# Optimization experiments

Measured on AMD Instinct MI355X. Metric: run time of the kernel, lower is better.

The kernel has to match this reference:

```python
import jax, jax.numpy as jnp
import numpy as np

B, N, X_DIM, Y_DIM = 256, 128, 8, 8
Z_DIM, R_DIM, HID = 64, 128, 256
STEPS = 50
SIGMA_SQ = 0.5 ** 2
EPSILON = 1.0


def setup_inputs() -> dict:
    key = jax.random.key(0)
    ks = jax.random.split(key, 20)
    s = lambda fan_in: 1.0 / np.sqrt(fan_in)
    inp = {
        'x_ctx': jax.random.normal(ks[0], (B, N, X_DIM), jnp.float32),
        'y_ctx': jax.random.normal(ks[1], (B, N, Y_DIM), jnp.float32),
        'mask': jnp.ones((B, N, 1), jnp.float32),
        'z0': jax.random.normal(ks[2], (B, Z_DIM), jnp.float32),
        'noise': jax.random.normal(ks[3], (STEPS, B, Z_DIM), jnp.float32),
        # encoder: pointwise MLP on [x,y] then masked mean pool, project to r_dim
        'We1': jax.random.normal(ks[4], (X_DIM + Y_DIM, HID), jnp.float32) * s(X_DIM + Y_DIM),
        'be1': jnp.zeros((HID,), jnp.float32),
        'We2': jax.random.normal(ks[5], (HID, R_DIM), jnp.float32) * s(HID),
        'be2': jnp.zeros((R_DIM,), jnp.float32),
        # decoder: MLP([x, z]) -> y per context point
        'Wd1': jax.random.normal(ks[6], (X_DIM + Z_DIM, HID), jnp.float32) * s(X_DIM + Z_DIM),
        'bd1': jnp.zeros((HID,), jnp.float32),
        'Wd2': jax.random.normal(ks[7], (HID, Y_DIM), jnp.float32) * s(HID),
        'bd2': jnp.zeros((Y_DIM,), jnp.float32),
        # drift net: MLP([z, r, t]) -> z_dim
        'Wb1': jax.random.normal(ks[8], (Z_DIM + R_DIM + 1, HID), jnp.float32) * s(Z_DIM + R_DIM + 1),
        'bb1': jnp.zeros((HID,), jnp.float32),
        'Wb2': jax.random.normal(ks[9], (HID, Z_DIM), jnp.float32) * s(HID),
        'bb2': jnp.zeros((Z_DIM,), jnp.float32),
    }
    return inp


def _encode(x, y, mask, We1, be1, We2, be2):
    phi = jax.nn.gelu(jnp.concatenate([x, y], axis=-1) @ We1 + be1)  # [B,N,H]
    pooled = (phi * mask).sum(axis=1) / jnp.maximum(mask.sum(axis=1), 1.0)  # [B,H]
    return pooled @ We2 + be2  # [B,R]


def _decode(z, x, Wd1, bd1, Wd2, bd2):
    zb = jnp.broadcast_to(z[:, None, :], (z.shape[0], x.shape[1], z.shape[1]))
    h = jax.nn.gelu(jnp.concatenate([x, zb], axis=-1) @ Wd1 + bd1)  # [B,N,H]
    return h @ Wd2 + bd2  # [B,N,Y]


def _drift(z, r, t_col, Wb1, bb1, Wb2, bb2):
    h = jax.nn.gelu(jnp.concatenate([z, r, t_col], axis=-1) @ Wb1 + bb1)
    return h @ Wb2 + bb2  # [B,Z]


def reference(x_ctx, y_ctx, mask, z0, noise,
              We1, be1, We2, be2, Wd1, bd1, Wd2, bd2, Wb1, bb1, Wb2, bb2):
    dt = 1.0 / STEPS
    r = _encode(x_ctx, y_ctx, mask, We1, be1, We2, be2)  # [B,R]

    def energy_sum(z, t):
        u0 = 0.5 * jnp.sum(z ** 2, axis=1)  # [B]
        mu_y = _decode(z, x_ctx, Wd1, bd1, Wd2, bd2)
        sse = jnp.sum(((y_ctx - mu_y) ** 2) * mask, axis=(1, 2))  # [B]
        u1 = 0.5 * sse / SIGMA_SQ + u0
        return jnp.sum((1.0 - t) * u0 + t * u1)

    grad_energy = jax.grad(energy_sum, argnums=0)
    t_steps = (jnp.arange(STEPS, dtype=jnp.float32) * dt)
    noise_scale = jnp.sqrt(jnp.float32(2.0 * EPSILON * dt))

    def step(z, xs):
        t_curr, eps_noise = xs
        grad_u = jnp.clip(grad_energy(z, t_curr), -100.0, 100.0)
        t_col = jnp.full((z.shape[0], 1), t_curr, dtype=z.dtype)
        b = _drift(z, r, t_col, Wb1, bb1, Wb2, bb2)
        dz = (-EPSILON * grad_u + b) * dt + noise_scale * eps_noise
        return z + dz, None

    z_final, _ = jax.lax.scan(step, z0, (t_steps, noise))
    return z_final
```

## Files before the change

kernel.cpp:

```cpp
#include <hip/hip_runtime.h>
#include <math.h>

#define BB    256
#define NN_   128
#define ZD    64
#define RD    128
#define HID   256
#define NSTEPS 50
#define NT    16
#define NTILES 8
#define TPB   1024
#define PADD  258
#define SPLIT 25

__device__ __forceinline__ double fast_exp_d(double x) {
    const double L2E   = 1.44269504088896340736;
    const double LN2HI = 6.93147180369123816490e-01;
    const double LN2LO = 1.90821492927058770002e-10;
    const double MAGIC = 6755399441055744.0;
    double vn = fma(x, L2E, MAGIC);
    int ni = __double2loint(vn);
    double n = vn - MAGIC;
    double r = fma(n, -LN2HI, x);
    r = fma(n, -LN2LO, r);
    double r2 = r * r;
    double r4 = r2 * r2;
    double p01 = 1.0 + r;
    double p23 = fma(r, 1.66666666666666666667e-01, 0.5);
    double p45 = fma(r, 8.33333333333333333333e-03, 4.16666666666666666667e-02);
    double p67 = fma(r, 1.98412698412698412698e-04, 1.38888888888888888889e-03);
    double p89 = fma(r, 2.75573192239858906526e-06, 2.48015873015873015873e-05);
    double pAB = fma(r, 2.50521083854417187751e-08, 2.75573192239858906526e-07);
    double q0 = fma(r2, p23, p01);
    double q1 = fma(r2, p67, p45);
    double q2 = fma(r2, pAB, p89);
    double p = fma(r4, fma(r4, q2, q1), q0);
    return p * __hiloint2double((1023 + ni) << 20, 0);
}

__device__ __forceinline__ double sigmoid_d(double w) {
    double wc = fmin(fmax(w, -60.0), 60.0);
    double e = fast_exp_d(-wc);
    double d = 1.0 + e;
    float r0 = __builtin_amdgcn_rcpf((float)d);
    double y = (double)r0;
    y = fma(y, fma(-d, y, 1.0), y);
    y = fma(y, fma(-d, y, 1.0), y);
    return y;
}

__device__ __forceinline__ double gelu_d(double x) {
    const double c2 = 1.59576912160573071176;
    double w = c2 * x * fma(0.044715, x * x, 1.0);
    return x * sigmoid_d(w);
}

__device__ __forceinline__ void gelu_both_d(double x, double& h, double& gp) {
    const double c  = 0.79788456080286535588;
    const double a  = 0.044715;
    double x2 = x * x;
    double w  = (2.0 * c) * x * fma(a, x2, 1.0);
    double hp = sigmoid_d(w);
    h = x * hp;
    double s = hp * (1.0 - hp);
    gp = fma(x * s, (2.0 * c) * fma(3.0 * a, x2, 1.0), hp);
}

__device__ __forceinline__ void gelu_both_f(float x, float& h, float& gp) {
    const float c2 = 1.5957691216f;
    float x2 = x * x;
    float w  = c2 * x * fmaf(0.044715f, x2, 1.0f);
    float e  = __expf(-w);
    float d  = 1.0f + e;
    float r0 = __builtin_amdgcn_rcpf(d);
    float hp = r0 * fmaf(-d, r0, 2.0f);
    h = x * hp;
    float sg = hp * (1.0f - hp);
    gp = fmaf(x * sg, c2 * fmaf(0.134145f, x2, 1.0f), hp);
}

__device__ __forceinline__ float gelu_f32(float x) {
    const float c2 = 1.5957691216f;
    float w  = c2 * x * fmaf(0.044715f, x * x, 1.0f);
    float e  = __expf(-w);
    float d  = 1.0f + e;
    float r0 = __builtin_amdgcn_rcpf(d);
    float hp = r0 * fmaf(-d, r0, 2.0f);
    return x * hp;
}

struct Smem {
    double h_t[NT][PADD];
    float  wd2t_f[8][PADD];
    double z_ds[ZD];
    double hb_ds[HID];
    double scratch4[4][HID];
    double pmgz[1024];
    double res_r[NT][8];
    double bp_d[16][ZD];
    double bd2_d[8];
    double bb2_d[ZD];
    double hbt_s[HID];
    double wbt_s[HID];
    float  bd1_s[HID];
    float  x_s[NN_][8];
    float  y_s[NN_][8];
    float  m_s[NN_];
    float  z_f[ZD];
    float  hb_f[HID];
    __align__(16) float4 wd1z4[HID][16];
};

__global__ void __launch_bounds__(TPB)
nets_sampler_kernel(
    const float* __restrict__ x_ctx, const float* __restrict__ y_ctx,
    const float* __restrict__ mask,  const float* __restrict__ z0,
    const float* __restrict__ noise,
    const float* __restrict__ We1, const float* __restrict__ be1,
    const float* __restrict__ We2, const float* __restrict__ be2,
    const float* __restrict__ Wd1, const float* __restrict__ bd1,
    const float* __restrict__ Wd2, const float* __restrict__ bd2,
    const float* __restrict__ Wb1, const float* __restrict__ bb1,
    const float* __restrict__ Wb2, const float* __restrict__ bb2,
    float* __restrict__ out)
{
    extern __shared__ char smem_raw[];
    Smem& sm = *reinterpret_cast<Smem*>(smem_raw);

    const int b   = blockIdx.x;
    const int tid = threadIdx.x;
    const int j   = tid & 255;
    const int q2  = tid >> 8;
    const int du_k = tid & 63, du_c = tid >> 6;
    double* r_d = &sm.res_r[0][0];

    if (tid < 256) {
        reinterpret_cast<float4*>(&sm.x_s[0][0])[tid] =
            reinterpret_cast<const float4*>(x_ctx + (size_t)b * NN_ * 8)[tid];
        reinterpret_cast<float4*>(&sm.y_s[0][0])[tid] =
            reinterpret_cast<const float4*>(y_ctx + (size_t)b * NN_ * 8)[tid];
        sm.bd1_s[j] = bd1[j];
        float4 a0 = reinterpret_cast<const float4*>(Wd2 + (size_t)j * 8)[0];
        float4 a1 = reinterpret_cast<const float4*>(Wd2 + (size_t)j * 8)[1];
        sm.wd2t_f[0][j] = a0.x; sm.wd2t_f[1][j] = a0.y;
        sm.wd2t_f[2][j] = a0.z; sm.wd2t_f[3][j] = a0.w;
        sm.wd2t_f[4][j] = a1.x; sm.wd2t_f[5][j] = a1.y;
        sm.wd2t_f[6][j] = a1.z; sm.wd2t_f[7][j] = a1.w;
    }
    if (tid < NN_) sm.m_s[tid] = mask[(size_t)b * NN_ + tid];
    if (tid < ZD) {
        float zf = z0[(size_t)b * ZD + tid];
        sm.z_ds[tid]  = (double)zf;
        sm.z_f[tid]   = zf;
        sm.bb2_d[tid] = (double)bb2[tid];
    }
    if (tid < 8) sm.bd2_d[tid] = (double)bd2[tid];

#pragma unroll
    for (int kk = 0; kk < 16; kk++) {
        const int k = q2 * 16 + kk;
        const float v = Wd1[(8 + k) * HID + j];
        reinterpret_cast<float*>(&sm.wd1z4[j][0])[4 * ((k >> 2) ^ (j & 15)) + (k & 3)] = v;
    }

    float wd1x[8];
#pragma unroll
    for (int k = 0; k < 8; k++) wd1x[k] = Wd1[k * HID + j];

    __syncthreads();

    if (tid < 256) {
        float we1r[16];
#pragma unroll
        for (int k = 0; k < 16; k++) we1r[k] = We1[k * HID + j];
        double be1_d = (double)be1[j];
        double msum = 0.0;
        for (int n = 0; n < NN_; n++) msum += (double)sm.m_s[n];
        msum = fmax(msum, 1.0);
        double pacc = 0.0;
        for (int n = 0; n < NN_; n++) {
            double pre = be1_d;
#pragma unroll
            for (int k = 0; k < 8; k++) pre = fma((double)sm.x_s[n][k], (double)we1r[k], pre);
#pragma unroll
            for (int k = 0; k < 8; k++) pre = fma((double)sm.y_s[n][k], (double)we1r[8 + k], pre);
            pacc += gelu_d(pre) * (double)sm.m_s[n];
        }
        sm.hb_ds[j] = pacc / msum;
    }
    __syncthreads();
    if (tid < 256) {
        int i = tid & 127, half = tid >> 7;
        double racc = 0.0;
        for (int jj = half * 128; jj < half * 128 + 128; jj++)
            racc = fma(sm.hb_ds[jj], (double)We2[jj * RD + i], racc);
        sm.scratch4[half][i] = racc;
    }
    __syncthreads();
    if (tid < RD) r_d[tid] = sm.scratch4[0][tid] + sm.scratch4[1][tid] + (double)be2[tid];
    __syncthreads();

    if (tid < 256) {
        double hbr = (double)bb1[j];
        for (int k = 0; k < RD; k++)
            hbr = fma(r_d[k], (double)Wb1[(ZD + k) * HID + j], hbr);
        sm.hbt_s[j] = hbr;
        sm.wbt_s[j] = (double)Wb1[(ZD + RD) * HID + j];
    }
    __syncthreads();

    const double dt  = 1.0 / (double)NSTEPS;
    const double nsc = sqrt(2.0 * 1.0 * dt);

    float* h_f   = reinterpret_cast<float*>(&sm.h_t[0][0]);
    float* res_f = reinterpret_cast<float*>(&sm.res_r[0][0]);
    float* pm_f  = reinterpret_cast<float*>(&sm.pmgz[0]);

    for (int s = 0; s < SPLIT; s++) {
        const double t = (double)s * dt;

        float nzf = 0.0f;
        if (tid < ZD) nzf = noise[((size_t)s * BB + b) * ZD + tid];

        {
            const int kb = q2 * 16;
            const float* wb1p = Wb1 + kb * HID + j;
            double a0 = 0.0;
#pragma unroll 8
            for (int kk = 0; kk < 16; kk++)
                a0 = fma(sm.z_ds[kb + kk], (double)wb1p[kk * HID], a0);
            sm.scratch4[q2][j] = a0;

            double zq0 = 0.0, zq1 = 0.0;
#pragma unroll
            for (int q = q2 * 4; q < q2 * 4 + 4; q++) {
                float4 wv = sm.wd1z4[j][q ^ (j & 15)];
                const int k = q * 4;
                zq0 = fma(sm.z_ds[k],     (double)wv.x, zq0);
                zq1 = fma(sm.z_ds[k + 1], (double)wv.y, zq1);
                zq0 = fma(sm.z_ds[k + 2], (double)wv.z, zq0);
                zq1 = fma(sm.z_ds[k + 3], (double)wv.w, zq1);
            }
            sm.pmgz[q2 * 256 + j] = zq0 + zq1;
        }
        __syncthreads();
        if (tid < 256) {
            double hacc = sm.hbt_s[j] + t * sm.wbt_s[j]
                        + sm.scratch4[0][j] + sm.scratch4[1][j]
                        + sm.scratch4[2][j] + sm.scratch4[3][j];
            sm.hb_ds[j] = gelu_d(hacc);
        }
        __syncthreads();
        {
            const float* wb2p = Wb2 + (du_c * 16) * ZD + du_k;
            double acc = 0.0;
#pragma unroll 8
            for (int i = 0; i < 16; i++)
                acc = fma(sm.hb_ds[du_c * 16 + i], (double)wb2p[i * ZD], acc);
            sm.bp_d[du_c][du_k] = acc;
        }

        if (s > 0) {
            const double zpre = (double)sm.bd1_s[j]
                + ((sm.pmgz[j] + sm.pmgz[256 + j]) + (sm.pmgz[512 + j] + sm.pmgz[768 + j]));
            const int rb = q2 * 4;

            float gp_r0, gp_r1, gp_r2, gp_r3;
            double T0 = 0.0, T1 = 0.0, T2 = 0.0, T3 = 0.0;
            double T4 = 0.0, T5 = 0.0, T6 = 0.0, T7 = 0.0;

            for (int tile = 0; tile < NTILES; tile++) {
                const int xb = tile * NT + rb;
                {
                    const float4 xa = *reinterpret_cast<const float4*>(&sm.x_s[xb + 0][0]);
                    const float4 xxb = *reinterpret_cast<const float4*>(&sm.x_s[xb + 0][4]);
                    const float4 xc = *reinterpret_cast<const float4*>(&sm.x_s[xb + 1][0]);
                    const float4 xd = *reinterpret_cast<const float4*>(&sm.x_s[xb + 1][4]);
                    double p0 = zpre, p1 = zpre;
                    p0 = fma((double)xa.x, (double)wd1x[0], p0);
                    p0 = fma((double)xa.y, (double)wd1x[1], p0);
                    p0 = fma((double)xa.z, (double)wd1x[2], p0);
                    p0 = fma((double)xa.w, (double)wd1x[3], p0);
                    p0 = fma((double)xxb.x, (double)wd1x[4], p0);
                    p0 = fma((double)xxb.y, (double)wd1x[5], p0);
                    p0 = fma((double)xxb.z, (double)wd1x[6], p0);
                    p0 = fma((double)xxb.w, (double)wd1x[7], p0);
                    p1 = fma((double)xc.x, (double)wd1x[0], p1);
                    p1 = fma((double)xc.y, (double)wd1x[1], p1);
                    p1 = fma((double)xc.z, (double)wd1x[2], p1);
                    p1 = fma((double)xc.w, (double)wd1x[3], p1);
                    p1 = fma((double)xd.x, (double)wd1x[4], p1);
                    p1 = fma((double)xd.y, (double)wd1x[5], p1);
                    p1 = fma((double)xd.z, (double)wd1x[6], p1);
                    p1 = fma((double)xd.w, (double)wd1x[7], p1);
                    double h0, g0, h1, g1;
                    gelu_both_d(p0, h0, g0);
                    gelu_both_d(p1, h1, g1);
                    sm.h_t[rb + 0][j] = h0; gp_r0 = (float)g0;
                    sm.h_t[rb + 1][j] = h1; gp_r1 = (float)g1;
                }
                {
                    const float4 xa = *reinterpret_cast<const float4*>(&sm.x_s[xb + 2][0]);
                    const float4 xxb = *reinterpret_cast<const float4*>(&sm.x_s[xb + 2][4]);
                    const float4 xc = *reinterpret_cast<const float4*>(&sm.x_s[xb + 3][0]);
                    const float4 xd = *reinterpret_cast<const float4*>(&sm.x_s[xb + 3][4]);
                    double p0 = zpre, p1 = zpre;
                    p0 = fma((double)xa.x, (double)wd1x[0], p0);
                    p0 = fma((double)xa.y, (double)wd1x[1], p0);
                    p0 = fma((double)xa.z, (double)wd1x[2], p0);
                    p0 = fma((double)xa.w, (double)wd1x[3], p0);
                    p0 = fma((double)xxb.x, (double)wd1x[4], p0);
                    p0 = fma((double)xxb.y, (double)wd1x[5], p0);
                    p0 = fma((double)xxb.z, (double)wd1x[6], p0);
                    p0 = fma((double)xxb.w, (double)wd1x[7], p0);
                    p1 = fma((double)xc.x, (double)wd1x[0], p1);
                    p1 = fma((double)xc.y, (double)wd1x[1], p1);
                    p1 = fma((double)xc.z, (double)wd1x[2], p1);
                    p1 = fma((double)xc.w, (double)wd1x[3], p1);
                    p1 = fma((double)xd.x, (double)wd1x[4], p1);
                    p1 = fma((double)xd.y, (double)wd1x[5], p1);
                    p1 = fma((double)xd.z, (double)wd1x[6], p1);
                    p1 = fma((double)xd.w, (double)wd1x[7], p1);
                    double h0, g0, h1, g1;
                    gelu_both_d(p0, h0, g0);
                    gelu_both_d(p1, h1, g1);
                    sm.h_t[rb + 2][j] = h0; gp_r2 = (float)g0;
                    sm.h_t[rb + 3][j] = h1; gp_r3 = (float)g1;
                }
                __syncthreads();
                {
                    const int q = tid >> 7, pair = tid & 127;
                    const int nn = pair >> 3, yd = pair & 7;
                    const double2* hrow = reinterpret_cast<const double2*>(&sm.h_t[nn][q * 32]);
                    const float2*  wrow = reinterpret_cast<const float2*>(&sm.wd2t_f[yd][q * 32]);
                    double a0 = 0.0, a1 = 0.0;
#pragma unroll 8
                    for (int i = 0; i < 16; i++) {
                        double2 hv = hrow[i];
                        float2  wv = wrow[i];
                        a0 = fma(hv.x, (double)wv.x, a0);
                        a1 = fma(hv.y, (double)wv.y, a1);
                    }
                    sm.pmgz[q * 128 + pair] = a0 + a1;
                }
                __syncthreads();
                if (tid < 128) {
                    const int nn = tid >> 3, yd = tid & 7;
                    double mu = sm.bd2_d[yd];
#pragma unroll
                    for (int q = 0; q < 8; q++) mu += sm.pmgz[q * 128 + tid];
                    sm.res_r[nn][yd] = 4.0 * t * (mu - (double)sm.y_s[tile * NT + nn][yd])
                                               * (double)sm.m_s[tile * NT + nn];
                }
                __syncthreads();
                {
                    const double2* rr0 = reinterpret_cast<const double2*>(&sm.res_r[rb + 0][0]);
                    const double2* rr1 = reinterpret_cast<const double2*>(&sm.res_r[rb + 1][0]);
                    const double2* rr2 = reinterpret_cast<const double2*>(&sm.res_r[rb + 2][0]);
                    const double2* rr3 = reinterpret_cast<const double2*>(&sm.res_r[rb + 3][0]);
                    double2 a0, a1, a2, a3;
                    double g;
                    g = (double)gp_r0;
                    a0 = rr0[0]; a1 = rr0[1]; a2 = rr0[2]; a3 = rr0[3];
                    T0 = fma(a0.x, g, T0); T1 = fma(a0.y, g, T1);
                    T2 = fma(a1.x, g, T2); T3 = fma(a1.y, g, T3);
                    T4 = fma(a2.x, g, T4); T5 = fma(a2.y, g, T5);
                    T6 = fma(a3.x, g, T6); T7 = fma(a3.y, g, T7);
                    g = (double)gp_r1;
                    a0 = rr1[0]; a1 = rr1[1]; a2 = rr1[2]; a3 = rr1[3];
                    T0 = fma(a0.x, g, T0); T1 = fma(a0.y, g, T1);
                    T2 = fma(a1.x, g, T2); T3 = fma(a1.y, g, T3);
                    T4 = fma(a2.x, g, T4); T5 = fma(a2.y, g, T5);
                    T6 = fma(a3.x, g, T6); T7 = fma(a3.y, g, T7);
                    g = (double)gp_r2;
                    a0 = rr2[0]; a1 = rr2[1]; a2 = rr2[2]; a3 = rr2[3];
                    T0 = fma(a0.x, g, T0); T1 = fma(a0.y, g, T1);
                    T2 = fma(a1.x, g, T2); T3 = fma(a1.y, g, T3);
                    T4 = fma(a2.x, g, T4); T5 = fma(a2.y, g, T5);
                    T6 = fma(a3.x, g, T6); T7 = fma(a3.y, g, T7);
                    g = (double)gp_r3;
                    a0 = rr3[0]; a1 = rr3[1]; a2 = rr3[2]; a3 = rr3[3];
                    T0 = fma(a0.x, g, T0); T1 = fma(a0.y, g, T1);
                    T2 = fma(a1.x, g, T2); T3 = fma(a1.y, g, T3);
                    T4 = fma(a2.x, g, T4); T5 = fma(a2.y, g, T5);
                    T6 = fma(a3.x, g, T6); T7 = fma(a3.y, g, T7);
                }
            }
            {
                double S = T0 * (double)sm.wd2t_f[0][j];
                S = fma(T1, (double)sm.wd2t_f[1][j], S);
                S = fma(T2, (double)sm.wd2t_f[2][j], S);
                S = fma(T3, (double)sm.wd2t_f[3][j], S);
                S = fma(T4, (double)sm.wd2t_f[4][j], S);
                S = fma(T5, (double)sm.wd2t_f[5][j], S);
                S = fma(T6, (double)sm.wd2t_f[6][j], S);
                S = fma(T7, (double)sm.wd2t_f[7][j], S);
                sm.scratch4[q2][j] = S;
            }
            __syncthreads();
            {
                const int k = du_k, c = du_c;
                const int qk = k >> 2, ck = k & 3;
                double acc = 0.0;
#pragma unroll 8
                for (int i = 0; i < 16; i++) {
                    const int jj = c * 16 + i;
                    const float w = reinterpret_cast<const float*>(&sm.wd1z4[jj][0])
                                        [4 * (qk ^ (jj & 15)) + ck];
                    const double sv = sm.scratch4[0][jj] + sm.scratch4[1][jj]
                                    + sm.scratch4[2][jj] + sm.scratch4[3][jj];
                    acc = fma(sv, (double)w, acc);
                }
                sm.pmgz[c * 64 + k] = acc;
            }
            __syncthreads();
        } else {
            __syncthreads();
        }

        if (tid < ZD) {
            double gsum = sm.z_ds[tid];
            if (s > 0) {
#pragma unroll
                for (int c = 0; c < 16; c++) gsum += sm.pmgz[c * 64 + tid];
            }
            gsum = fmin(fmax(gsum, -100.0), 100.0);
            double bdr = sm.bb2_d[tid];
#pragma unroll
            for (int c = 0; c < 16; c++) bdr += sm.bp_d[c][tid];
            double znew = sm.z_ds[tid] + (bdr - gsum) * dt + nsc * (double)nzf;
            sm.z_ds[tid] = znew;
            sm.z_f[tid]  = (float)znew;
        }
        __syncthreads();
    }

    for (int s = SPLIT; s < NSTEPS; s++) {
        const double t = (double)s * dt;

        float nzf = 0.0f;
        if (tid < ZD) nzf = noise[((size_t)s * BB + b) * ZD + tid];

        {
            const int kb = q2 * 16;
            const float* wb1p = Wb1 + kb * HID + j;
            float a0f = 0.0f;
#pragma unroll 8
            for (int kk = 0; kk < 16; kk++)
                a0f = fmaf(sm.z_f[kb + kk], wb1p[kk * HID], a0f);
            sm.scratch4[q2][j] = (double)a0f;

            double zq0 = 0.0, zq1 = 0.0;
#pragma unroll
            for (int q = q2 * 4; q < q2 * 4 + 4; q++) {
                float4 wv = sm.wd1z4[j][q ^ (j & 15)];
                const int k = q * 4;
                zq0 = fma(sm.z_ds[k],     (double)wv.x, zq0);
                zq1 = fma(sm.z_ds[k + 1], (double)wv.y, zq1);
                zq0 = fma(sm.z_ds[k + 2], (double)wv.z, zq0);
                zq1 = fma(sm.z_ds[k + 3], (double)wv.w, zq1);
            }
            sm.pmgz[q2 * 256 + j] = zq0 + zq1;
        }
        __syncthreads();
        if (tid < 256) {
            double hacc = sm.hbt_s[j] + t * sm.wbt_s[j]
                        + sm.scratch4[0][j] + sm.scratch4[1][j]
                        + sm.scratch4[2][j] + sm.scratch4[3][j];
            sm.hb_f[j] = gelu_f32((float)hacc);
        }
        __syncthreads();
        {
            const float* wb2p = Wb2 + (du_c * 16) * ZD + du_k;
            float accf = 0.0f;
#pragma unroll 8
            for (int i = 0; i < 16; i++)
                accf = fmaf(sm.hb_f[du_c * 16 + i], wb2p[i * ZD], accf);
            sm.bp_d[du_c][du_k] = (double)accf;
        }

        const double zpre = (double)sm.bd1_s[j]
            + ((sm.pmgz[j] + sm.pmgz[256 + j]) + (sm.pmgz[512 + j] + sm.pmgz[768 + j]));
        const float zpre_f = (float)zpre;
        const int rb2 = q2 * 8;

        float gpA, gpB, gpC, gpD, gpE, gpF2, gpG, gpH;
        float T0 = 0.f, T1 = 0.f, T2 = 0.f, T3 = 0.f;
        float T4 = 0.f, T5 = 0.f, T6 = 0.f, T7 = 0.f;

        for (int tile = 0; tile < 4; tile++) {
            const int xb = tile * 32 + rb2;
#define FPAIR(RO, GA, GB) { \
            const float4 xa = *reinterpret_cast<const float4*>(&sm.x_s[xb + (RO)][0]); \
            const float4 xbv = *reinterpret_cast<const float4*>(&sm.x_s[xb + (RO)][4]); \
            const float4 xc = *reinterpret_cast<const float4*>(&sm.x_s[xb + (RO) + 1][0]); \
            const float4 xdv = *reinterpret_cast<const float4*>(&sm.x_s[xb + (RO) + 1][4]); \
            float p0 = zpre_f, p1 = zpre_f; \
            p0 = fmaf(xa.x, wd1x[0], p0);  p0 = fmaf(xa.y, wd1x[1], p0); \
            p0 = fmaf(xa.z, wd1x[2], p0);  p0 = fmaf(xa.w, wd1x[3], p0); \
            p0 = fmaf(xbv.x, wd1x[4], p0); p0 = fmaf(xbv.y, wd1x[5], p0); \
            p0 = fmaf(xbv.z, wd1x[6], p0); p0 = fmaf(xbv.w, wd1x[7], p0); \
            p1 = fmaf(xc.x, wd1x[0], p1);  p1 = fmaf(xc.y, wd1x[1], p1); \
            p1 = fmaf(xc.z, wd1x[2], p1);  p1 = fmaf(xc.w, wd1x[3], p1); \
            p1 = fmaf(xdv.x, wd1x[4], p1); p1 = fmaf(xdv.y, wd1x[5], p1); \
            p1 = fmaf(xdv.z, wd1x[6], p1); p1 = fmaf(xdv.w, wd1x[7], p1); \
            float h0, g0, h1, g1; \
            gelu_both_f(p0, h0, g0); \
            gelu_both_f(p1, h1, g1); \
            h_f[(rb2 + (RO)) * PADD + j]     = h0; \
            h_f[(rb2 + (RO) + 1) * PADD + j] = h1; \
            GA = g0; GB = g1; }
            FPAIR(0, gpA, gpB)
            FPAIR(2, gpC, gpD)
            FPAIR(4, gpE, gpF2)
            FPAIR(6, gpG, gpH)
#undef FPAIR
            __syncthreads();
#pragma unroll
            for (int it = 0; it < 2; it++) {
                const int slot = tid + it * 1024;
                const int q = slot >> 8, pair = slot & 255;
                const int nn = pair >> 3, yd = pair & 7;
                const float2* hrow =
                    reinterpret_cast<const float2*>(h_f + nn * PADD) + q * 16;
                const float2* wrow =
                    reinterpret_cast<const float2*>(&sm.wd2t_f[yd][0]) + q * 16;
                float a0 = 0.f, a1 = 0.f;
#pragma unroll 8
                for (int i = 0; i < 16; i++) {
                    float2 hv = hrow[i];
                    float2 wv = wrow[i];
                    a0 = fmaf(hv.x, wv.x, a0);
                    a1 = fmaf(hv.y, wv.y, a1);
                }
                pm_f[slot] = a0 + a1;
            }
            __syncthreads();
            if (tid < 256) {
                const int nn = tid >> 3, yd = tid & 7;
                double mu = sm.bd2_d[yd];
#pragma unroll
                for (int q = 0; q < 8; q++) mu += (double)pm_f[q * 256 + tid];
                const int row = tile * 32 + nn;
                res_f[tid] = (float)(4.0 * t * (mu - (double)sm.y_s[row][yd])
                                             * (double)sm.m_s[row]);
            }
            __syncthreads();
#define BROW(RO, G) { \
            const float2* rr = reinterpret_cast<const float2*>(res_f + (rb2 + (RO)) * 8); \
            float2 a0 = rr[0], a1 = rr[1], a2 = rr[2], a3 = rr[3]; \
            T0 = fmaf(a0.x, (G), T0); T1 = fmaf(a0.y, (G), T1); \
            T2 = fmaf(a1.x, (G), T2); T3 = fmaf(a1.y, (G), T3); \
            T4 = fmaf(a2.x, (G), T4); T5 = fmaf(a2.y, (G), T5); \
            T6 = fmaf(a3.x, (G), T6); T7 = fmaf(a3.y, (G), T7); }
            BROW(0, gpA) BROW(1, gpB) BROW(2, gpC) BROW(3, gpD)
            BROW(4, gpE) BROW(5, gpF2) BROW(6, gpG) BROW(7, gpH)
#undef BROW
        }
        {
            float Sf = T0 * sm.wd2t_f[0][j];
            Sf = fmaf(T1, sm.wd2t_f[1][j], Sf);
            Sf = fmaf(T2, sm.wd2t_f[2][j], Sf);
            Sf = fmaf(T3, sm.wd2t_f[3][j], Sf);
            Sf = fmaf(T4, sm.wd2t_f[4][j], Sf);
            Sf = fmaf(T5, sm.wd2t_f[5][j], Sf);
            Sf = fmaf(T6, sm.wd2t_f[6][j], Sf);
            Sf = fmaf(T7, sm.wd2t_f[7][j], Sf);
            sm.scratch4[q2][j] = (double)Sf;
        }
        __syncthreads();

        {
            const int k = du_k, c = du_c;
            const int qk = k >> 2, ck = k & 3;
            double acc = 0.0;
#pragma unroll 8
            for (int i = 0; i < 16; i++) {
                const int jj = c * 16 + i;
                const float w = reinterpret_cast<const float*>(&sm.wd1z4[jj][0])
                                    [4 * (qk ^ (jj & 15)) + ck];
                const double sv = sm.scratch4[0][jj] + sm.scratch4[1][jj]
                                + sm.scratch4[2][jj] + sm.scratch4[3][jj];
                acc = fma(sv, (double)w, acc);
            }
            sm.pmgz[c * 64 + k] = acc;
        }
        __syncthreads();
        if (tid < ZD) {
            double gsum = sm.z_ds[tid];
#pragma unroll
            for (int c = 0; c < 16; c++) gsum += sm.pmgz[c * 64 + tid];
            gsum = fmin(fmax(gsum, -100.0), 100.0);
            double bdr = sm.bb2_d[tid];
#pragma unroll
            for (int c = 0; c < 16; c++) bdr += sm.bp_d[c][tid];
            double znew = sm.z_ds[tid] + (bdr - gsum) * dt + nsc * (double)nzf;
            sm.z_ds[tid] = znew;
            sm.z_f[tid]  = (float)znew;
        }
        __syncthreads();
    }

    if (tid < ZD) out[(size_t)b * ZD + tid] = (float)sm.z_ds[tid];
}

extern "C" void kernel_launch(void* const* d_in, const int* in_sizes, int n_in,
                              void* d_out, int out_size, void* d_ws, size_t ws_size,
                              hipStream_t stream) {
    const float* x_ctx = (const float*)d_in[0];
    const float* y_ctx = (const float*)d_in[1];
    const float* maskp = (const float*)d_in[2];
    const float* z0    = (const float*)d_in[3];
    const float* noise = (const float*)d_in[4];
    const float* We1   = (const float*)d_in[5];
    const float* be1   = (const float*)d_in[6];
    const float* We2   = (const float*)d_in[7];
    const float* be2   = (const float*)d_in[8];
    const float* Wd1   = (const float*)d_in[9];
    const float* bd1   = (const float*)d_in[10];
    const float* Wd2   = (const float*)d_in[11];
    const float* bd2   = (const float*)d_in[12];
    const float* Wb1   = (const float*)d_in[13];
    const float* bb1   = (const float*)d_in[14];
    const float* Wb2   = (const float*)d_in[15];
    const float* bb2   = (const float*)d_in[16];
    float* out = (float*)d_out;

    (void)hipFuncSetAttribute((const void*)nets_sampler_kernel,
                              hipFuncAttributeMaxDynamicSharedMemorySize,
                              (int)sizeof(Smem));

    nets_sampler_kernel<<<BB, TPB, sizeof(Smem), stream>>>(
        x_ctx, y_ctx, maskp, z0, noise,
        We1, be1, We2, be2, Wd1, bd1, Wd2, bd2, Wb1, bb1, Wb2, bb2, out);
}
```

Measured before the change: 1.508 ms.

## Software-pipeline decoder tile loop to cut barriers per tile

```diff
diff --git a/kernel.cpp b/kernel.cpp
--- a/kernel.cpp
+++ b/kernel.cpp
@@ -265,127 +265,145 @@
                 + ((sm.pmgz[j] + sm.pmgz[256 + j]) + (sm.pmgz[512 + j] + sm.pmgz[768 + j]));
             const int rb = q2 * 4;
 
-            float gp_r0, gp_r1, gp_r2, gp_r3;
+            float c0, c1, c2, c3;
+            float n0, n1, n2, n3;
             double T0 = 0.0, T1 = 0.0, T2 = 0.0, T3 = 0.0;
             double T4 = 0.0, T5 = 0.0, T6 = 0.0, T7 = 0.0;
 
-            for (int tile = 0; tile < NTILES; tile++) {
-                const int xb = tile * NT + rb;
-                {
-                    const float4 xa = *reinterpret_cast<const float4*>(&sm.x_s[xb + 0][0]);
-                    const float4 xxb = *reinterpret_cast<const float4*>(&sm.x_s[xb + 0][4]);
-                    const float4 xc = *reinterpret_cast<const float4*>(&sm.x_s[xb + 1][0]);
-                    const float4 xd = *reinterpret_cast<const float4*>(&sm.x_s[xb + 1][4]);
-                    double p0 = zpre, p1 = zpre;
-                    p0 = fma((double)xa.x, (double)wd1x[0], p0);
-                    p0 = fma((double)xa.y, (double)wd1x[1], p0);
-                    p0 = fma((double)xa.z, (double)wd1x[2], p0);
-                    p0 = fma((double)xa.w, (double)wd1x[3], p0);
-                    p0 = fma((double)xxb.x, (double)wd1x[4], p0);
-                    p0 = fma((double)xxb.y, (double)wd1x[5], p0);
-                    p0 = fma((double)xxb.z, (double)wd1x[6], p0);
-                    p0 = fma((double)xxb.w, (double)wd1x[7], p0);
-                    p1 = fma((double)xc.x, (double)wd1x[0], p1);
-                    p1 = fma((double)xc.y, (double)wd1x[1], p1);
-                    p1 = fma((double)xc.z, (double)wd1x[2], p1);
-                    p1 = fma((double)xc.w, (double)wd1x[3], p1);
-                    p1 = fma((double)xd.x, (double)wd1x[4], p1);
-                    p1 = fma((double)xd.y, (double)wd1x[5], p1);
-                    p1 = fma((double)xd.z, (double)wd1x[6], p1);
-                    p1 = fma((double)xd.w, (double)wd1x[7], p1);
-                    double h0, g0, h1, g1;
-                    gelu_both_d(p0, h0, g0);
-                    gelu_both_d(p1, h1, g1);
-                    sm.h_t[rb + 0][j] = h0; gp_r0 = (float)g0;
-                    sm.h_t[rb + 1][j] = h1; gp_r1 = (float)g1;
-                }
-                {
-                    const float4 xa = *reinterpret_cast<const float4*>(&sm.x_s[xb + 2][0]);
-                    const float4 xxb = *reinterpret_cast<const float4*>(&sm.x_s[xb + 2][4]);
-                    const float4 xc = *reinterpret_cast<const float4*>(&sm.x_s[xb + 3][0]);
-                    const float4 xd = *reinterpret_cast<const float4*>(&sm.x_s[xb + 3][4]);
-                    double p0 = zpre, p1 = zpre;
-                    p0 = fma((double)xa.x, (double)wd1x[0], p0);
-                    p0 = fma((double)xa.y, (double)wd1x[1], p0);
-                    p0 = fma((double)xa.z, (double)wd1x[2], p0);
-                    p0 = fma((double)xa.w, (double)wd1x[3], p0);
-                    p0 = fma((double)xxb.x, (double)wd1x[4], p0);
-                    p0 = fma((double)xxb.y, (double)wd1x[5], p0);
-                    p0 = fma((double)xxb.z, (double)wd1x[6], p0);
-                    p0 = fma((double)xxb.w, (double)wd1x[7], p0);
-                    p1 = fma((double)xc.x, (double)wd1x[0], p1);
-                    p1 = fma((double)xc.y, (double)wd1x[1], p1);
-                    p1 = fma((double)xc.z, (double)wd1x[2], p1);
-                    p1 = fma((double)xc.w, (double)wd1x[3], p1);
-                    p1 = fma((double)xd.x, (double)wd1x[4], p1);
-                    p1 = fma((double)xd.y, (double)wd1x[5], p1);
-                    p1 = fma((double)xd.z, (double)wd1x[6], p1);
-                    p1 = fma((double)xd.w, (double)wd1x[7], p1);
-                    double h0, g0, h1, g1;
-                    gelu_both_d(p0, h0, g0);
-                    gelu_both_d(p1, h1, g1);
-                    sm.h_t[rb + 2][j] = h0; gp_r2 = (float)g0;
-                    sm.h_t[rb + 3][j] = h1; gp_r3 = (float)g1;
-                }
+#define FA(TI, G0, G1, G2, G3) { \
+            const int xb = (TI) * NT + rb; \
+            { \
+                const float4 xa = *reinterpret_cast<const float4*>(&sm.x_s[xb + 0][0]); \
+                const float4 xbv = *reinterpret_cast<const float4*>(&sm.x_s[xb + 0][4]); \
+                const float4 xc = *reinterpret_cast<const float4*>(&sm.x_s[xb + 1][0]); \
+                const float4 xdv = *reinterpret_cast<const float4*>(&sm.x_s[xb + 1][4]); \
+                double p0 = zpre, p1 = zpre; \
+                p0 = fma((double)xa.x, (double)wd1x[0], p0); \
+                p0 = fma((double)xa.y, (double)wd1x[1], p0); \
+                p0 = fma((double)xa.z, (double)wd1x[2], p0); \
+                p0 = fma((double)xa.w, (double)wd1x[3], p0); \
+                p0 = fma((double)xbv.x, (double)wd1x[4], p0); \
+                p0 = fma((double)xbv.y, (double)wd1x[5], p0); \
+                p0 = fma((double)xbv.z, (double)wd1x[6], p0); \
+                p0 = fma((double)xbv.w, (double)wd1x[7], p0); \
+                p1 = fma((double)xc.x, (double)wd1x[0], p1); \
+                p1 = fma((double)xc.y, (double)wd1x[1], p1); \
+                p1 = fma((double)xc.z, (double)wd1x[2], p1); \
+                p1 = fma((double)xc.w, (double)wd1x[3], p1); \
+                p1 = fma((double)xdv.x, (double)wd1x[4], p1); \
+                p1 = fma((double)xdv.y, (double)wd1x[5], p1); \
+                p1 = fma((double)xdv.z, (double)wd1x[6], p1); \
+                p1 = fma((double)xdv.w, (double)wd1x[7], p1); \
+                double h0, g0, h1, g1; \
+                gelu_both_d(p0, h0, g0); \
+                gelu_both_d(p1, h1, g1); \
+                sm.h_t[rb + 0][j] = h0; G0 = (float)g0; \
+                sm.h_t[rb + 1][j] = h1; G1 = (float)g1; \
+            } \
+            { \
+                const float4 xa = *reinterpret_cast<const float4*>(&sm.x_s[xb + 2][0]); \
+                const float4 xbv = *reinterpret_cast<const float4*>(&sm.x_s[xb + 2][4]); \
+                const float4 xc = *reinterpret_cast<const float4*>(&sm.x_s[xb + 3][0]); \
+                const float4 xdv = *reinterpret_cast<const float4*>(&sm.x_s[xb + 3][4]); \
+                double p0 = zpre, p1 = zpre; \
+                p0 = fma((double)xa.x, (double)wd1x[0], p0); \
+                p0 = fma((double)xa.y, (double)wd1x[1], p0); \
+                p0 = fma((double)xa.z, (double)wd1x[2], p0); \
+                p0 = fma((double)xa.w, (double)wd1x[3], p0); \
+                p0 = fma((double)xbv.x, (double)wd1x[4], p0); \
+                p0 = fma((double)xbv.y, (double)wd1x[5], p0); \
+                p0 = fma((double)xbv.z, (double)wd1x[6], p0); \
+                p0 = fma((double)xbv.w, (double)wd1x[7], p0); \
+                p1 = fma((double)xc.x, (double)wd1x[0], p1); \
+                p1 = fma((double)xc.y, (double)wd1x[1], p1); \
+                p1 = fma((double)xc.z, (double)wd1x[2], p1); \
+                p1 = fma((double)xc.w, (double)wd1x[3], p1); \
+                p1 = fma((double)xdv.x, (double)wd1x[4], p1); \
+                p1 = fma((double)xdv.y, (double)wd1x[5], p1); \
+                p1 = fma((double)xdv.z, (double)wd1x[6], p1); \
+                p1 = fma((double)xdv.w, (double)wd1x[7], p1); \
+                double h0, g0, h1, g1; \
+                gelu_both_d(p0, h0, g0); \
+                gelu_both_d(p1, h1, g1); \
+                sm.h_t[rb + 2][j] = h0; G2 = (float)g0; \
+                sm.h_t[rb + 3][j] = h1; G3 = (float)g1; \
+            } }
+
+#define MA() { \
+            const int q = tid >> 7, pair = tid & 127; \
+            const int nn = pair >> 3, yd = pair & 7; \
+            const double2* hrow = reinterpret_cast<const double2*>(&sm.h_t[nn][q * 32]); \
+            const float2*  wrow = reinterpret_cast<const float2*>(&sm.wd2t_f[yd][q * 32]); \
+            double a0 = 0.0, a1 = 0.0; \
+            _Pragma("unroll 8") \
+            for (int i = 0; i < 16; i++) { \
+                double2 hv = hrow[i]; \
+                float2  wv = wrow[i]; \
+                a0 = fma(hv.x, (double)wv.x, a0); \
+                a1 = fma(hv.y, (double)wv.y, a1); \
+            } \
+            sm.pmgz[q * 128 + pair] = a0 + a1; }
+
+#define RA(TI) if (tid < 128) { \
+            const int nn = tid >> 3, yd = tid & 7; \
+            double mu = sm.bd2_d[yd]; \
+            _Pragma("unroll") \
+            for (int q = 0; q < 8; q++) mu += sm.pmgz[q * 128 + tid]; \
+            sm.res_r[nn][yd] = 4.0 * t * (mu - (double)sm.y_s[(TI) * NT + nn][yd]) \
+                                       * (double)sm.m_s[(TI) * NT + nn]; }
+
+#define BA(G0, G1, G2, G3) { \
+            const double2* rr0 = reinterpret_cast<const double2*>(&sm.res_r[rb + 0][0]); \
+            const double2* rr1 = reinterpret_cast<const double2*>(&sm.res_r[rb + 1][0]); \
+            const double2* rr2 = reinterpret_cast<const double2*>(&sm.res_r[rb + 2][0]); \
+            const double2* rr3 = reinterpret_cast<const double2*>(&sm.res_r[rb + 3][0]); \
+            double2 a0, a1, a2, a3; \
+            double g; \
+            g = (double)G0; \
+            a0 = rr0[0]; a1 = rr0[1]; a2 = rr0[2]; a3 = rr0[3]; \
+            T0 = fma(a0.x, g, T0); T1 = fma(a0.y, g, T1); \
+            T2 = fma(a1.x, g, T2); T3 = fma(a1.y, g, T3); \
+            T4 = fma(a2.x, g, T4); T5 = fma(a2.y, g, T5); \
+            T6 = fma(a3.x, g, T6); T7 = fma(a3.y, g, T7); \
+            g = (double)G1; \
+            a0 = rr1[0]; a1 = rr1[1]; a2 = rr1[2]; a3 = rr1[3]; \
+            T0 = fma(a0.x, g, T0); T1 = fma(a0.y, g, T1); \
+            T2 = fma(a1.x, g, T2); T3 = fma(a1.y, g, T3); \
+            T4 = fma(a2.x, g, T4); T5 = fma(a2.y, g, T5); \
+            T6 = fma(a3.x, g, T6); T7 = fma(a3.y, g, T7); \
+            g = (double)G2; \
+            a0 = rr2[0]; a1 = rr2[1]; a2 = rr2[2]; a3 = rr2[3]; \
+            T0 = fma(a0.x, g, T0); T1 = fma(a0.y, g, T1); \
+            T2 = fma(a1.x, g, T2); T3 = fma(a1.y, g, T3); \
+            T4 = fma(a2.x, g, T4); T5 = fma(a2.y, g, T5); \
+            T6 = fma(a3.x, g, T6); T7 = fma(a3.y, g, T7); \
+            g = (double)G3; \
+            a0 = rr3[0]; a1 = rr3[1]; a2 = rr3[2]; a3 = rr3[3]; \
+            T0 = fma(a0.x, g, T0); T1 = fma(a0.y, g, T1); \
+            T2 = fma(a1.x, g, T2); T3 = fma(a1.y, g, T3); \
+            T4 = fma(a2.x, g, T4); T5 = fma(a2.y, g, T5); \
+            T6 = fma(a3.x, g, T6); T7 = fma(a3.y, g, T7); }
+
+            FA(0, c0, c1, c2, c3)
+            __syncthreads();
+            MA()
+            __syncthreads();
+            for (int k = 0; k < NTILES - 1; k++) {
+                RA(k)
+                FA(k + 1, n0, n1, n2, n3)
                 __syncthreads();
-                {
-                    const int q = tid >> 7, pair = tid & 127;
-                    const int nn = pair >> 3, yd = pair & 7;
-                    const double2* hrow = reinterpret_cast<const double2*>(&sm.h_t[nn][q * 32]);
-                    const float2*  wrow = reinterpret_cast<const float2*>(&sm.wd2t_f[yd][q * 32]);
-                    double a0 = 0.0, a1 = 0.0;
-#pragma unroll 8
-                    for (int i = 0; i < 16; i++) {
-                        double2 hv = hrow[i];
-                        float2  wv = wrow[i];
-                        a0 = fma(hv.x, (double)wv.x, a0);
-                        a1 = fma(hv.y, (double)wv.y, a1);
-                    }
-                    sm.pmgz[q * 128 + pair] = a0 + a1;
-                }
+                BA(c0, c1, c2, c3)
+                MA()
                 __syncthreads();
-                if (tid < 128) {
-                    const int nn = tid >> 3, yd = tid & 7;
-                    double mu = sm.bd2_d[yd];
-#pragma unroll
-                    for (int q = 0; q < 8; q++) mu += sm.pmgz[q * 128 + tid];
-                    sm.res_r[nn][yd] = 4.0 * t * (mu - (double)sm.y_s[tile * NT + nn][yd])
-                                               * (double)sm.m_s[tile * NT + nn];
-                }
-                __syncthreads();
-                {
-                    const double2* rr0 = reinterpret_cast<const double2*>(&sm.res_r[rb + 0][0]);
-                    const double2* rr1 = reinterpret_cast<const double2*>(&sm.res_r[rb + 1][0]);
-                    const double2* rr2 = reinterpret_cast<const double2*>(&sm.res_r[rb + 2][0]);
-                    const double2* rr3 = reinterpret_cast<const double2*>(&sm.res_r[rb + 3][0]);
-                    double2 a0, a1, a2, a3;
-                    double g;
-                    g = (double)gp_r0;
-                    a0 = rr0[0]; a1 = rr0[1]; a2 = rr0[2]; a3 = rr0[3];
-                    T0 = fma(a0.x, g, T0); T1 = fma(a0.y, g, T1);
-                    T2 = fma(a1.x, g, T2); T3 = fma(a1.y, g, T3);
-                    T4 = fma(a2.x, g, T4); T5 = fma(a2.y, g, T5);
-                    T6 = fma(a3.x, g, T6); T7 = fma(a3.y, g, T7);
-                    g = (double)gp_r1;
-                    a0 = rr1[0]; a1 = rr1[1]; a2 = rr1[2]; a3 = rr1[3];
-                    T0 = fma(a0.x, g, T0); T1 = fma(a0.y, g, T1);
-                    T2 = fma(a1.x, g, T2); T3 = fma(a1.y, g, T3);
-                    T4 = fma(a2.x, g, T4); T5 = fma(a2.y, g, T5);
-                    T6 = fma(a3.x, g, T6); T7 = fma(a3.y, g, T7);
-                    g = (double)gp_r2;
-                    a0 = rr2[0]; a1 = rr2[1]; a2 = rr2[2]; a3 = rr2[3];
-                    T0 = fma(a0.x, g, T0); T1 = fma(a0.y, g, T1);
-                    T2 = fma(a1.x, g, T2); T3 = fma(a1.y, g, T3);
-                    T4 = fma(a2.x, g, T4); T5 = fma(a2.y, g, T5);
-                    T6 = fma(a3.x, g, T6); T7 = fma(a3.y, g, T7);
-                    g = (double)gp_r3;
-                    a0 = rr3[0]; a1 = rr3[1]; a2 = rr3[2]; a3 = rr3[3];
-                    T0 = fma(a0.x, g, T0); T1 = fma(a0.y, g, T1);
-                    T2 = fma(a1.x, g, T2); T3 = fma(a1.y, g, T3);
-                    T4 = fma(a2.x, g, T4); T5 = fma(a2.y, g, T5);
-                    T6 = fma(a3.x, g, T6); T7 = fma(a3.y, g, T7);
-                }
+                c0 = n0; c1 = n1; c2 = n2; c3 = n3;
             }
+            RA(NTILES - 1)
+            __syncthreads();
+            BA(c0, c1, c2, c3)
+#undef FA
+#undef MA
+#undef RA
+#undef BA
             {
                 double S = T0 * (double)sm.wd2t_f[0][j];
                 S = fma(T1, (double)sm.wd2t_f[1][j], S);
@@ -484,79 +502,104 @@
         const float zpre_f = (float)zpre;
         const int rb2 = q2 * 8;
 
-        float gpA, gpB, gpC, gpD, gpE, gpF2, gpG, gpH;
+        float cA, cB, cC, cD, cE, cF, cG, cH;
+        float nA, nB, nC, nD, nE, nF, nG, nH;
         float T0 = 0.f, T1 = 0.f, T2 = 0.f, T3 = 0.f;
         float T4 = 0.f, T5 = 0.f, T6 = 0.f, T7 = 0.f;
 
-        for (int tile = 0; tile < 4; tile++) {
-            const int xb = tile * 32 + rb2;
-#define FPAIR(RO, GA, GB) { \
-            const float4 xa = *reinterpret_cast<const float4*>(&sm.x_s[xb + (RO)][0]); \
-            const float4 xbv = *reinterpret_cast<const float4*>(&sm.x_s[xb + (RO)][4]); \
-            const float4 xc = *reinterpret_cast<const float4*>(&sm.x_s[xb + (RO) + 1][0]); \
-            const float4 xdv = *reinterpret_cast<const float4*>(&sm.x_s[xb + (RO) + 1][4]); \
-            float p0 = zpre_f, p1 = zpre_f; \
-            p0 = fmaf(xa.x, wd1x[0], p0);  p0 = fmaf(xa.y, wd1x[1], p0); \
-            p0 = fmaf(xa.z, wd1x[2], p0);  p0 = fmaf(xa.w, wd1x[3], p0); \
-            p0 = fmaf(xbv.x, wd1x[4], p0); p0 = fmaf(xbv.y, wd1x[5], p0); \
-            p0 = fmaf(xbv.z, wd1x[6], p0); p0 = fmaf(xbv.w, wd1x[7], p0); \
-            p1 = fmaf(xc.x, wd1x[0], p1);  p1 = fmaf(xc.y, wd1x[1], p1); \
-            p1 = fmaf(xc.z, wd1x[2], p1);  p1 = fmaf(xc.w, wd1x[3], p1); \
-            p1 = fmaf(xdv.x, wd1x[4], p1); p1 = fmaf(xdv.y, wd1x[5], p1); \
-            p1 = fmaf(xdv.z, wd1x[6], p1); p1 = fmaf(xdv.w, wd1x[7], p1); \
-            float h0, g0, h1, g1; \
-            gelu_both_f(p0, h0, g0); \
-            gelu_both_f(p1, h1, g1); \
-            h_f[(rb2 + (RO)) * PADD + j]     = h0; \
-            h_f[(rb2 + (RO) + 1) * PADD + j] = h1; \
-            GA = g0; GB = g1; }
-            FPAIR(0, gpA, gpB)
-            FPAIR(2, gpC, gpD)
-            FPAIR(4, gpE, gpF2)
-            FPAIR(6, gpG, gpH)
+#define FPAIR(XB, RO, GA, GB) { \
+        const float4 xa = *reinterpret_cast<const float4*>(&sm.x_s[(XB) + (RO)][0]); \
+        const float4 xbv = *reinterpret_cast<const float4*>(&sm.x_s[(XB) + (RO)][4]); \
+        const float4 xc = *reinterpret_cast<const float4*>(&sm.x_s[(XB) + (RO) + 1][0]); \
+        const float4 xdv = *reinterpret_cast<const float4*>(&sm.x_s[(XB) + (RO) + 1][4]); \
+        float p0 = zpre_f, p1 = zpre_f; \
+        p0 = fmaf(xa.x, wd1x[0], p0);  p0 = fmaf(xa.y, wd1x[1], p0); \
+        p0 = fmaf(xa.z, wd1x[2], p0);  p0 = fmaf(xa.w, wd1x[3], p0); \
+        p0 = fmaf(xbv.x, wd1x[4], p0); p0 = fmaf(xbv.y, wd1x[5], p0); \
+        p0 = fmaf(xbv.z, wd1x[6], p0); p0 = fmaf(xbv.w, wd1x[7], p0); \
+        p1 = fmaf(xc.x, wd1x[0], p1);  p1 = fmaf(xc.y, wd1x[1], p1); \
+        p1 = fmaf(xc.z, wd1x[2], p1);  p1 = fmaf(xc.w, wd1x[3], p1); \
+        p1 = fmaf(xdv.x, wd1x[4], p1); p1 = fmaf(xdv.y, wd1x[5], p1); \
+        p1 = fmaf(xdv.z, wd1x[6], p1); p1 = fmaf(xdv.w, wd1x[7], p1); \
+        float h0, g0, h1, g1; \
+        gelu_both_f(p0, h0, g0); \
+        gelu_both_f(p1, h1, g1); \
+        h_f[(rb2 + (RO)) * PADD + j]     = h0; \
+        h_f[(rb2 + (RO) + 1) * PADD + j] = h1; \
+        GA = g0; GB = g1; }
+
+#define FB(TI, GA, GB, GC, GD, GE, GF, GG, GH) { \
+        const int xb = (TI) * 32 + rb2; \
+        FPAIR(xb, 0, GA, GB) \
+        FPAIR(xb, 2, GC, GD) \
+        FPAIR(xb, 4, GE, GF) \
+        FPAIR(xb, 6, GG, GH) }
+
+#define MB() { \
+        _Pragma("unroll") \
+        for (int it = 0; it < 2; it++) { \
+            const int slot = tid + it * 1024; \
+            const int q = slot >> 8, pair = slot & 255; \
+            const int nn = pair >> 3, yd = pair & 7; \
+            const float2* hrow = \
+                reinterpret_cast<const float2*>(h_f + nn * PADD) + q * 16; \
+            const float2* wrow = \
+                reinterpret_cast<const float2*>(&sm.wd2t_f[yd][0]) + q * 16; \
+            float a0 = 0.f, a1 = 0.f; \
+            _Pragma("unroll 8") \
+            for (int i = 0; i < 16; i++) { \
+                float2 hv = hrow[i]; \
+                float2 wv = wrow[i]; \
+                a0 = fmaf(hv.x, wv.x, a0); \
+                a1 = fmaf(hv.y, wv.y, a1); \
+            } \
+            pm_f[slot] = a0 + a1; \
+        } }
+
+#define RB(TI) if (tid < 256) { \
+        const int nn = tid >> 3, yd = tid & 7; \
+        double mu = sm.bd2_d[yd]; \
+        _Pragma("unroll") \
+        for (int q = 0; q < 8; q++) mu += (double)pm_f[q * 256 + tid]; \
+        const int row = (TI) * 32 + nn; \
+        res_f[tid] = (float)(4.0 * t * (mu - (double)sm.y_s[row][yd]) \
+                                     * (double)sm.m_s[row]); }
+
+#define BROW(RO, G) { \
+        const float2* rr = reinterpret_cast<const float2*>(res_f + (rb2 + (RO)) * 8); \
+        float2 a0 = rr[0], a1 = rr[1], a2 = rr[2], a3 = rr[3]; \
+        T0 = fmaf(a0.x, (G), T0); T1 = fmaf(a0.y, (G), T1); \
+        T2 = fmaf(a1.x, (G), T2); T3 = fmaf(a1.y, (G), T3); \
+        T4 = fmaf(a2.x, (G), T4); T5 = fmaf(a2.y, (G), T5); \
+        T6 = fmaf(a3.x, (G), T6); T7 = fmaf(a3.y, (G), T7); }
+
+#define BBLK(GA, GB, GC, GD, GE, GF, GG, GH) { \
+        BROW(0, GA) BROW(1, GB) BROW(2, GC) BROW(3, GD) \
+        BROW(4, GE) BROW(5, GF) BROW(6, GG) BROW(7, GH) }
+
+        FB(0, cA, cB, cC, cD, cE, cF, cG, cH)
+        __syncthreads();
+        MB()
+        __syncthreads();
+        for (int k = 0; k < 3; k++) {
+            RB(k)
+            FB(k + 1, nA, nB, nC, nD, nE, nF, nG, nH)
+            __syncthreads();
+            BBLK(cA, cB, cC, cD, cE, cF, cG, cH)
+            MB()
+            __syncthreads();
+            cA = nA; cB = nB; cC = nC; cD = nD;
+            cE = nE; cF = nF; cG = nG; cH = nH;
+        }
+        RB(3)
+        __syncthreads();
+        BBLK(cA, cB, cC, cD, cE, cF, cG, cH)
 #undef FPAIR
-            __syncthreads();
-#pragma unroll
-            for (int it = 0; it < 2; it++) {
-                const int slot = tid + it * 1024;
-                const int q = slot >> 8, pair = slot & 255;
-                const int nn = pair >> 3, yd = pair & 7;
-                const float2* hrow =
-                    reinterpret_cast<const float2*>(h_f + nn * PADD) + q * 16;
-                const float2* wrow =
-                    reinterpret_cast<const float2*>(&sm.wd2t_f[yd][0]) + q * 16;
-                float a0 = 0.f, a1 = 0.f;
-#pragma unroll 8
-                for (int i = 0; i < 16; i++) {
-                    float2 hv = hrow[i];
-                    float2 wv = wrow[i];
-                    a0 = fmaf(hv.x, wv.x, a0);
-                    a1 = fmaf(hv.y, wv.y, a1);
-                }
-                pm_f[slot] = a0 + a1;
-            }
-            __syncthreads();
-            if (tid < 256) {
-                const int nn = tid >> 3, yd = tid & 7;
-                double mu = sm.bd2_d[yd];
-#pragma unroll
-                for (int q = 0; q < 8; q++) mu += (double)pm_f[q * 256 + tid];
-                const int row = tile * 32 + nn;
-                res_f[tid] = (float)(4.0 * t * (mu - (double)sm.y_s[row][yd])
-                                             * (double)sm.m_s[row]);
-            }
-            __syncthreads();
-#define BROW(RO, G) { \
-            const float2* rr = reinterpret_cast<const float2*>(res_f + (rb2 + (RO)) * 8); \
-            float2 a0 = rr[0], a1 = rr[1], a2 = rr[2], a3 = rr[3]; \
-            T0 = fmaf(a0.x, (G), T0); T1 = fmaf(a0.y, (G), T1); \
-            T2 = fmaf(a1.x, (G), T2); T3 = fmaf(a1.y, (G), T3); \
-            T4 = fmaf(a2.x, (G), T4); T5 = fmaf(a2.y, (G), T5); \
-            T6 = fmaf(a3.x, (G), T6); T7 = fmaf(a3.y, (G), T7); }
-            BROW(0, gpA) BROW(1, gpB) BROW(2, gpC) BROW(3, gpD)
-            BROW(4, gpE) BROW(5, gpF2) BROW(6, gpG) BROW(7, gpH)
+#undef FB
+#undef MB
+#undef RB
 #undef BROW
-        }
+#undef BBLK
         {
             float Sf = T0 * sm.wd2t_f[0][j];
             Sf = fmaf(T1, sm.wd2t_f[1][j], Sf);
```

Result: slower. 3.522 ms (+133.5%).
